# Kernel optimization log

Hardware: AMD Instinct MI355X
Metric: run time of the kernel (lower is better)

## Reference

```python
import jax, jax.numpy as jnp
import numpy as np
from math import erf, pi, sqrt, exp

D = 2048
TARGET_BITS = 2.5
N_HIGH = 1024  # round(D * frac)
N_LOW = D - N_HIGH
HIGH_MSE_BITS = 2  # ceil(2.5) - 1
LOW_MSE_BITS = 1   # floor(2.5) - 1


def _phi(x):
    return np.exp(-0.5 * x * x) / np.sqrt(2.0 * np.pi)


def _Phi(x):
    return 0.5 * (1.0 + np.vectorize(erf)(x / np.sqrt(2.0)))


def lloyd_max_centroids(bits: int) -> np.ndarray:
    """Lloyd-Max optimal scalar quantizer centroids for N(0,1), 2**bits levels."""
    L = 2 ** bits
    c = np.linspace(-2.0, 2.0, L)
    for _ in range(200):
        b = 0.5 * (c[:-1] + c[1:])                      # decision boundaries
        edges = np.concatenate([[-1e9], b, [1e9]])
        lo, hi = edges[:-1], edges[1:]
        mass = _Phi(hi) - _Phi(lo)
        c = (_phi(lo) - _phi(hi)) / np.maximum(mass, 1e-12)  # conditional mean
    return c.astype(np.float32)


def generate_rotation_matrix(d: int, seed: int) -> np.ndarray:
    rng = np.random.default_rng(seed)
    A = rng.standard_normal((d, d)).astype(np.float64)
    Q, R = np.linalg.qr(A)
    Q = Q * np.sign(np.diag(R))[None, :]
    return Q.astype(np.float32)


def setup_inputs() -> dict:
    key = jax.random.key(0)
    kq, kk = jax.random.split(key)
    queries = jax.random.normal(kq, (1024, D), dtype=jnp.float32)
    keys = jax.random.normal(kk, (4096, D), dtype=jnp.float32)
    Pi = jnp.asarray(generate_rotation_matrix(D, seed=42 + 2000))
    high_centroids = jnp.asarray(lloyd_max_centroids(HIGH_MSE_BITS))  # (4,)
    low_centroids = jnp.asarray(lloyd_max_centroids(LOW_MSE_BITS))    # (2,)
    rng = np.random.default_rng(42)
    S_high = jnp.asarray(rng.standard_normal((N_HIGH, N_HIGH)).astype(np.float32))
    rng2 = np.random.default_rng(42 + 1000)
    S_low = jnp.asarray(rng2.standard_normal((N_LOW, N_LOW)).astype(np.float32))
    return {"queries": queries, "keys": keys, "Pi": Pi,
            "high_centroids": high_centroids, "low_centroids": low_centroids,
            "S_high": S_high, "S_low": S_low}


def _quantize_group(y, centroids, S):
    # nearest-centroid scalar quantization per channel
    idx = jnp.argmin(jnp.abs(y[..., None] - centroids), axis=-1)  # (bk, n_ch)
    y_mse = centroids[idx]
    residual = y - y_mse
    residual_norm = jnp.linalg.norm(residual, axis=-1)            # (bk,)
    signs = jnp.sign(residual @ S.T)                              # (bk, m)
    return y_mse, signs, residual_norm


def _ip_group(q_ch, y_mse, signs, residual_norm, S):
    m = S.shape[0]
    term1 = q_ch @ y_mse.T                                        # (bq, bk)
    # QJL estimator: <q, r> ~ sqrt(pi/2)/m * ||r|| * <S q, sign(S r)>
    term2 = (jnp.sqrt(jnp.float32(pi / 2)) / m) * ((q_ch @ S.T) @ signs.T) * residual_norm[None, :]
    return term1 + term2


def reference(queries, keys, Pi, high_centroids, low_centroids, S_high, S_low):
    # ---- quantize keys ----
    vec_norm = jnp.linalg.norm(keys, axis=-1)                     # (bk,)
    k_n = keys / (vec_norm[:, None] + 1e-8)
    y = k_n @ Pi.T
    yh, yl = y[:, :N_HIGH], y[:, N_HIGH:]
    kmse_h, sg_h, rn_h = _quantize_group(yh, high_centroids, S_high)
    kmse_l, sg_l, rn_l = _quantize_group(yl, low_centroids, S_low)
    # ---- inner product estimate ----
    q_rot = queries @ Pi.T
    qh, ql = q_rot[:, :N_HIGH], q_rot[:, N_HIGH:]
    ip = _ip_group(qh, kmse_h, sg_h, rn_h, S_high) + _ip_group(ql, kmse_l, sg_l, rn_l, S_low)
    return ip * vec_norm[None, :]                                 # (bq, bk)
```

## Files before the change

### kernel.cpp

```cpp
#include <hip/hip_runtime.h>
#include <math.h>

#ifndef M_PI
#define M_PI 3.14159265358979323846
#endif

typedef __attribute__((ext_vector_type(8))) __bf16 bf16x8;
typedef __attribute__((ext_vector_type(4))) float f32x4;
typedef __attribute__((ext_vector_type(8))) unsigned short ushort8;
typedef __attribute__((ext_vector_type(4))) unsigned short ushort4v;

__device__ __forceinline__ unsigned short f2bf(float x) {
    unsigned int u = __float_as_uint(x);
    unsigned int r = (u + 0x7FFFu + ((u >> 16) & 1u)) >> 16;
    return (unsigned short)r;
}

__global__ __launch_bounds__(256)
void norm_np_k(const float* __restrict__ keys,
               float* __restrict__ den,
               float* __restrict__ vnorm)
{
#pragma clang fp contract(off)
    const int tid = threadIdx.x;
    const int row_l = tid >> 4;
    const int blk = tid & 15;
    const int row = blockIdx.x * 16 + row_l;
    const float* a = keys + (size_t)row * 2048 + blk * 128;

    float r0 = a[0]*a[0], r1 = a[1]*a[1], r2 = a[2]*a[2], r3 = a[3]*a[3];
    float r4 = a[4]*a[4], r5 = a[5]*a[5], r6 = a[6]*a[6], r7 = a[7]*a[7];
    for (int i = 8; i < 128; i += 8) {
        r0 += a[i+0]*a[i+0]; r1 += a[i+1]*a[i+1];
        r2 += a[i+2]*a[i+2]; r3 += a[i+3]*a[i+3];
        r4 += a[i+4]*a[i+4]; r5 += a[i+5]*a[i+5];
        r6 += a[i+6]*a[i+6]; r7 += a[i+7]*a[i+7];
    }
    float bsum = ((r0 + r1) + (r2 + r3)) + ((r4 + r5) + (r6 + r7));

    __shared__ float bs[16][16];
    bs[row_l][blk] = bsum;
    __syncthreads();
    if (blk == 0) {
        const float* b = bs[row_l];
        float q0 = ((b[0] + b[1]) + (b[2] + b[3])) + ((b[4] + b[5]) + (b[6] + b[7]));
        float q1 = ((b[8] + b[9]) + (b[10] + b[11])) + ((b[12] + b[13]) + (b[14] + b[15]));
        float s = q0 + q1;
        float n = (float)sqrt((double)s);
        den[row] = n + 1e-8f;
        vnorm[row] = n;
    }
}

__global__ __launch_bounds__(256)
void kn_k(const float* __restrict__ keys,
          const float* __restrict__ den,
          float* __restrict__ kn)
{
#pragma clang fp contract(off)
    const int idx = (blockIdx.x * 256 + threadIdx.x) * 8;
    const int row = idx >> 11;
    const float d = den[row];
    float4 v0 = *(const float4*)(keys + idx);
    float4 v1 = *(const float4*)(keys + idx + 4);
    v0.x /= d; v0.y /= d; v0.z /= d; v0.w /= d;
    v1.x /= d; v1.y /= d; v1.z /= d; v1.w /= d;
    *(float4*)(kn + idx) = v0;
    *(float4*)(kn + idx + 4) = v1;
}

__global__ __launch_bounds__(256)
void f2bf_k(const float* __restrict__ in, unsigned short* __restrict__ out)
{
    const int i = (blockIdx.x * 256 + threadIdx.x) * 8;
    float4 v0 = *(const float4*)(in + i);
    float4 v1 = *(const float4*)(in + i + 4);
    ushort8 o;
    o[0] = f2bf(v0.x); o[1] = f2bf(v0.y); o[2] = f2bf(v0.z); o[3] = f2bf(v0.w);
    o[4] = f2bf(v1.x); o[5] = f2bf(v1.y); o[6] = f2bf(v1.z); o[7] = f2bf(v1.w);
    *(ushort8*)(out + i) = o;
}

template <int EPI>
__global__ __launch_bounds__(256)
void gemm_dec_k(const float* __restrict__ A, int lda, int a_zoff,
                const float* __restrict__ B0, const float* __restrict__ B1,
                int ldb,
                float* __restrict__ Cf, unsigned short* __restrict__ Cb,
                int c_zoff, int ldc, int K,
                const float* __restrict__ rv0, const float* __restrict__ rv1)
{
#pragma clang fp contract(off)
    __shared__ float As[16][132];
    __shared__ float Bs[16][132];

    const int z = blockIdx.z;
    const float* Ap = A + (size_t)z * a_zoff;
    const float* Bp = z ? B1 : B0;
    const float* rvp = z ? rv1 : rv0;
    unsigned short* Cbp = (EPI == 1) ? (Cb + (size_t)z * c_zoff) : nullptr;

    const int tid = threadIdx.x;
    const int tr4 = (tid >> 4) * 4;
    const int tc4 = (tid & 15) * 4;
    const int row0 = blockIdx.y * 128;
    const int col0 = blockIdx.x * 128;
    const int sr = tid >> 1;
    const int sk = (tid & 1) * 8;

    const float* ga = Ap + (size_t)(row0 + sr) * lda + sk;
    const float* gb = Bp + (size_t)(col0 + sr) * ldb + sk;

    float acc[2][2][4][4] = {};
    float sa[8], sb[8];

#define LOADSTAGE(off) do { \
    *(float4*)(sa)     = *(const float4*)(ga + (off)); \
    *(float4*)(sa + 4) = *(const float4*)(ga + (off) + 4); \
    *(float4*)(sb)     = *(const float4*)(gb + (off)); \
    *(float4*)(sb + 4) = *(const float4*)(gb + (off) + 4); \
} while (0)

#define RDFRAG(fa, fb, kk) do { \
    *(float4*)(fa)     = *(const float4*)&As[kk][tr4]; \
    *(float4*)(fa + 4) = *(const float4*)&As[kk][tr4 + 64]; \
    *(float4*)(fb)     = *(const float4*)&Bs[kk][tc4]; \
    *(float4*)(fb + 4) = *(const float4*)&Bs[kk][tc4 + 64]; \
} while (0)

#define FMAS(fa, fb) do { \
    _Pragma("unroll") \
    for (int mb = 0; mb < 2; ++mb) \
        _Pragma("unroll") \
        for (int i = 0; i < 4; ++i) \
            _Pragma("unroll") \
            for (int nb = 0; nb < 2; ++nb) \
                _Pragma("unroll") \
                for (int j = 0; j < 4; ++j) \
                    acc[mb][nb][i][j] = fmaf((fa)[mb*4+i], (fb)[nb*4+j], acc[mb][nb][i][j]); \
} while (0)

    LOADSTAGE(0);

    for (int k0 = 0; k0 < K; k0 += 16) {
        __syncthreads();
        #pragma unroll
        for (int u = 0; u < 8; ++u) {
            As[sk + u][sr] = sa[u];
            Bs[sk + u][sr] = sb[u];
        }
        __syncthreads();
        if (k0 + 16 < K) LOADSTAGE(k0 + 16);

        float fa0[8], fb0[8], fa1[8], fb1[8];
        RDFRAG(fa0, fb0, 0);
        #pragma unroll
        for (int kk = 0; kk < 16; kk += 2) {
            RDFRAG(fa1, fb1, kk + 1);
            FMAS(fa0, fb0);
            if (kk + 2 < 16) RDFRAG(fa0, fb0, kk + 2);
            FMAS(fa1, fb1);
        }
    }

    #pragma unroll
    for (int mb = 0; mb < 2; ++mb) {
        #pragma unroll
        for (int i = 0; i < 4; ++i) {
            const int r = row0 + mb * 64 + tr4 + i;
            if (EPI == 0) {
                #pragma unroll
                for (int nb = 0; nb < 2; ++nb)
                    *(float4*)&Cf[(size_t)r * ldc + col0 + nb * 64 + tc4] =
                        *(const float4*)&acc[mb][nb][i][0];
            } else {
                const float s = rvp[r];
                #pragma unroll
                for (int nb = 0; nb < 2; ++nb) {
                    ushort4v o;
                    #pragma unroll
                    for (int j = 0; j < 4; ++j) {
                        const float t = acc[mb][nb][i][j];
                        o[j] = f2bf((t > 0.0f) ? s : ((t < 0.0f) ? -s : 0.0f));
                    }
                    *(ushort4v*)&Cbp[(size_t)r * ldc + col0 + nb * 64 + tc4] = o;
                }
            }
        }
    }
#undef LOADSTAGE
#undef RDFRAG
#undef FMAS
}

__global__ __launch_bounds__(256)
void quant_k(float* __restrict__ Y,
             unsigned short* __restrict__ Bmse,
             const float* __restrict__ ch,
             const float* __restrict__ cl,
             float* __restrict__ sc_h,
             float* __restrict__ sc_l,
             double coefd)
{
#pragma clang fp contract(off)
    const int row = blockIdx.x;
    const int tid = threadIdx.x;
    const int c0 = tid * 8;
    const float h0 = ch[0], h1 = ch[1], h2 = ch[2], h3 = ch[3];
    const float l0 = cl[0], l1 = cl[1];

    float y[8], res[8];
    ushort8 cb;
    *(float4*)(y)     = *(const float4*)(Y + (size_t)row * 2048 + c0);
    *(float4*)(y + 4) = *(const float4*)(Y + (size_t)row * 2048 + c0 + 4);

    const bool high = (tid < 128);
    float ss = 0.0f;
    #pragma unroll
    for (int j = 0; j < 8; ++j) {
        const float v = y[j];
        float cbest;
        if (high) {
            cbest = h0;
            float bd = fabsf(v - h0), dd;
            dd = fabsf(v - h1); if (dd < bd) { bd = dd; cbest = h1; }
            dd = fabsf(v - h2); if (dd < bd) { bd = dd; cbest = h2; }
            dd = fabsf(v - h3); if (dd < bd) { bd = dd; cbest = h3; }
        } else {
            cbest = (fabsf(v - l1) < fabsf(v - l0)) ? l1 : l0;
        }
        res[j] = v - cbest;
        cb[j] = f2bf(cbest);
        ss += res[j] * res[j];
    }
    *(float4*)(Y + (size_t)row * 2048 + c0)     = *(float4*)(res);
    *(float4*)(Y + (size_t)row * 2048 + c0 + 4) = *(float4*)(res + 4);
    *(ushort8*)(Bmse + (size_t)row * 4096 + c0) = cb;

    __shared__ float sm[256];
    sm[tid] = ss;
    __syncthreads();
    for (int o = 64; o > 0; o >>= 1) {
        if ((tid & 127) < o) sm[tid] += sm[tid + o];
        __syncthreads();
    }
    if (tid == 0)   sc_h[row] = (float)(coefd * sqrt((double)sm[0]));
    if (tid == 128) sc_l[row] = (float)(coefd * sqrt((double)sm[128]));
}

template <int EPI>
__global__ __launch_bounds__(256)
void gemm_mfma_k(const unsigned short* __restrict__ A, int lda, int a_zoff,
                 const unsigned short* __restrict__ B0,
                 const unsigned short* __restrict__ B1, int ldb,
                 float* __restrict__ Cf, unsigned short* __restrict__ Cb,
                 int c_zoff, int ldc, int K,
                 const float* __restrict__ colscale)
{
    __shared__ unsigned short As[128][40];
    __shared__ unsigned short Bs[128][40];

    const int z = blockIdx.z;
    const unsigned short* Ap = A + (size_t)z * a_zoff;
    const unsigned short* Bp = z ? B1 : B0;
    unsigned short* Cbp = (EPI == 2) ? (Cb + (size_t)z * c_zoff) : nullptr;

    const int tid = threadIdx.x;
    const int lane = tid & 63;
    const int wid = tid >> 6;
    const int wm = wid >> 1;
    const int wn = wid & 1;
    const int row0 = blockIdx.y * 128;
    const int col0 = blockIdx.x * 128;
    const int sr = tid >> 1;
    const int sk = (tid & 1) * 16;
    const int frow = lane & 15;
    const int fk = (lane >> 4) * 8;

    const unsigned short* ga = Ap + (size_t)(row0 + sr) * lda + sk;
    const unsigned short* gb = Bp + (size_t)(col0 + sr) * ldb + sk;

    f32x4 acc[4][4] = {};

    for (int k0 = 0; k0 < K; k0 += 32) {
        ushort8 a0 = *(const ushort8*)(ga + k0);
        ushort8 a1 = *(const ushort8*)(ga + k0 + 8);
        ushort8 b0 = *(const ushort8*)(gb + k0);
        ushort8 b1 = *(const ushort8*)(gb + k0 + 8);
        __syncthreads();
        *(ushort8*)&As[sr][sk]     = a0;
        *(ushort8*)&As[sr][sk + 8] = a1;
        *(ushort8*)&Bs[sr][sk]     = b0;
        *(ushort8*)&Bs[sr][sk + 8] = b1;
        __syncthreads();

        bf16x8 af[4], bfr[4];
        #pragma unroll
        for (int mi = 0; mi < 4; ++mi)
            af[mi] = *(const bf16x8*)&As[wm * 64 + mi * 16 + frow][fk];
        #pragma unroll
        for (int ni = 0; ni < 4; ++ni)
            bfr[ni] = *(const bf16x8*)&Bs[wn * 64 + ni * 16 + frow][fk];
        #pragma unroll
        for (int mi = 0; mi < 4; ++mi)
            #pragma unroll
            for (int ni = 0; ni < 4; ++ni)
                acc[mi][ni] = __builtin_amdgcn_mfma_f32_16x16x32_bf16(
                    af[mi], bfr[ni], acc[mi][ni], 0, 0, 0);
    }

    const int drow = (lane >> 4) * 4;
    const int dcol = lane & 15;
    #pragma unroll
    for (int mi = 0; mi < 4; ++mi) {
        #pragma unroll
        for (int ni = 0; ni < 4; ++ni) {
            const int c = col0 + wn * 64 + ni * 16 + dcol;
            const float cs = (EPI == 1) ? colscale[c] : 0.0f;
            #pragma unroll
            for (int rg = 0; rg < 4; ++rg) {
                const int r = row0 + wm * 64 + mi * 16 + drow + rg;
                const float v = acc[mi][ni][rg];
                if (EPI == 1) Cf[(size_t)r * ldc + c] = v * cs;
                else          Cbp[(size_t)r * ldc + c] = f2bf(v);
            }
        }
    }
}

extern "C" void kernel_launch(void* const* d_in, const int* in_sizes, int n_in,
                              void* d_out, int out_size, void* d_ws, size_t ws_size,
                              hipStream_t stream)
{
    const float* queries = (const float*)d_in[0];
    const float* keys    = (const float*)d_in[1];
    const float* Pi      = (const float*)d_in[2];
    const float* ch      = (const float*)d_in[3];
    const float* cl      = (const float*)d_in[4];
    const float* S_high  = (const float*)d_in[5];
    const float* S_low   = (const float*)d_in[6];
    float* out = (float*)d_out;

    char* ws = (char*)d_ws;
    float*          kn    = (float*)(ws);
    float*          Y     = (float*)(ws + ((size_t)32 << 20));
    unsigned short* Bbig  = (unsigned short*)(ws + ((size_t)64 << 20));
    unsigned short* Abig  = (unsigned short*)(ws + ((size_t)96 << 20));
    unsigned short* Qb    = (unsigned short*)(ws + ((size_t)104 << 20));
    unsigned short* Pib   = (unsigned short*)(ws + ((size_t)108 << 20));
    unsigned short* Sbh   = (unsigned short*)(ws + ((size_t)116 << 20));
    unsigned short* Sbl   = (unsigned short*)(ws + ((size_t)118 << 20));
    float*          den   = (float*)(ws + ((size_t)120 << 20));
    float*          vnorm = (float*)(ws + ((size_t)120 << 20) + 16384);
    float*          sc_h  = (float*)(ws + ((size_t)120 << 20) + 32768);
    float*          sc_l  = (float*)(ws + ((size_t)120 << 20) + 49152);

    const double coefd = sqrt(M_PI / 2.0) / 1024.0;

    norm_np_k<<<256, 256, 0, stream>>>(keys, den, vnorm);

    kn_k<<<4096, 256, 0, stream>>>(keys, den, kn);

    f2bf_k<<<1024, 256, 0, stream>>>(queries, Qb);
    f2bf_k<<<2048, 256, 0, stream>>>(Pi, Pib);
    f2bf_k<<<512, 256, 0, stream>>>(S_high, Sbh);
    f2bf_k<<<512, 256, 0, stream>>>(S_low, Sbl);

    gemm_dec_k<0><<<dim3(16, 32, 1), 256, 0, stream>>>(
        kn, 2048, 0, Pi, Pi, 2048, Y, nullptr, 0, 2048, 2048, nullptr, nullptr);

    quant_k<<<4096, 256, 0, stream>>>(Y, Bbig, ch, cl, sc_h, sc_l, coefd);

    gemm_dec_k<1><<<dim3(8, 32, 2), 256, 0, stream>>>(
        Y, 2048, 1024, S_high, S_low, 1024,
        nullptr, Bbig + 2048, 1024, 4096, 1024, sc_h, sc_l);

    gemm_mfma_k<2><<<dim3(16, 8, 1), 256, 0, stream>>>(
        Qb, 2048, 0, Pib, Pib, 2048, nullptr, Abig, 0, 4096, 2048, nullptr);
    gemm_mfma_k<2><<<dim3(8, 8, 2), 256, 0, stream>>>(
        Abig, 4096, 1024, Sbh, Sbl, 1024, nullptr, Abig + 2048, 1024, 4096, 1024, nullptr);

    gemm_mfma_k<1><<<dim3(32, 8, 1), 256, 0, stream>>>(
        Abig, 4096, 0, Bbig, Bbig, 4096, out, nullptr, 0, 4096, 4096, vnorm);
}
```

Before: 829.2 us.

## Double-buffer LDS tiles and use packed FP32 FMA in the fp32 GEMM

The fp32 SIMT GEMM now keeps two LDS buffers, so the next K-slice is written to the alternate buffer after compute and only one barrier is needed per iteration instead of two. The inner product loop is rewritten with inline v_pk_fma_f32 asm, where each instruction updates two accumulators, which roughly halves the FMA instruction count. The risks are doubled LDS use, which may lower occupancy, and inline asm that can block compiler scheduling. Rounding stays the same because each result is still a single fused multiply-add.

```diff
diff --git a/kernel.cpp b/kernel.cpp
--- a/kernel.cpp
+++ b/kernel.cpp
@@ -7,6 +7,7 @@
 
 typedef __attribute__((ext_vector_type(8))) __bf16 bf16x8;
 typedef __attribute__((ext_vector_type(4))) float f32x4;
+typedef __attribute__((ext_vector_type(2))) float f32x2;
 typedef __attribute__((ext_vector_type(8))) unsigned short ushort8;
 typedef __attribute__((ext_vector_type(4))) unsigned short ushort4v;
 
@@ -15,6 +16,13 @@
     unsigned int r = (u + 0x7FFFu + ((u >> 16) & 1u)) >> 16;
     return (unsigned short)r;
 }
+
+#define PKFMA_L(d, a, b) \
+    asm("v_pk_fma_f32 %0, %1, %2, %0 op_sel:[0,0,0] op_sel_hi:[0,1,1]" \
+        : "+v"(d) : "v"(a), "v"(b))
+#define PKFMA_H(d, a, b) \
+    asm("v_pk_fma_f32 %0, %1, %2, %0 op_sel:[1,0,0] op_sel_hi:[1,1,1]" \
+        : "+v"(d) : "v"(a), "v"(b))
 
 __global__ __launch_bounds__(256)
 void norm_np_k(const float* __restrict__ keys,
@@ -91,8 +99,8 @@
                 const float* __restrict__ rv0, const float* __restrict__ rv1)
 {
 #pragma clang fp contract(off)
-    __shared__ float As[16][132];
-    __shared__ float Bs[16][132];
+    __shared__ float As[2][16][132];
+    __shared__ float Bs[2][16][132];
 
     const int z = blockIdx.z;
     const float* Ap = A + (size_t)z * a_zoff;
@@ -111,7 +119,7 @@
     const float* ga = Ap + (size_t)(row0 + sr) * lda + sk;
     const float* gb = Bp + (size_t)(col0 + sr) * ldb + sk;
 
-    float acc[2][2][4][4] = {};
+    f32x2 acc[8][4] = {};
     float sa[8], sb[8];
 
 #define LOADSTAGE(off) do { \
@@ -121,74 +129,86 @@
     *(float4*)(sb + 4) = *(const float4*)(gb + (off) + 4); \
 } while (0)
 
-#define RDFRAG(fa, fb, kk) do { \
-    *(float4*)(fa)     = *(const float4*)&As[kk][tr4]; \
-    *(float4*)(fa + 4) = *(const float4*)&As[kk][tr4 + 64]; \
-    *(float4*)(fb)     = *(const float4*)&Bs[kk][tc4]; \
-    *(float4*)(fb + 4) = *(const float4*)&Bs[kk][tc4 + 64]; \
+#define STORESTAGE(buf) do { \
+    _Pragma("unroll") \
+    for (int u = 0; u < 8; ++u) { \
+        As[buf][sk + u][sr] = sa[u]; \
+        Bs[buf][sk + u][sr] = sb[u]; \
+    } \
+} while (0)
+
+#define RDFRAG(fa, fb, kk, buf) do { \
+    float4 va0 = *(const float4*)&As[buf][kk][tr4]; \
+    float4 va1 = *(const float4*)&As[buf][kk][tr4 + 64]; \
+    float4 vb0 = *(const float4*)&Bs[buf][kk][tc4]; \
+    float4 vb1 = *(const float4*)&Bs[buf][kk][tc4 + 64]; \
+    (fa)[0] = (f32x2){va0.x, va0.y}; (fa)[1] = (f32x2){va0.z, va0.w}; \
+    (fa)[2] = (f32x2){va1.x, va1.y}; (fa)[3] = (f32x2){va1.z, va1.w}; \
+    (fb)[0] = (f32x2){vb0.x, vb0.y}; (fb)[1] = (f32x2){vb0.z, vb0.w}; \
+    (fb)[2] = (f32x2){vb1.x, vb1.y}; (fb)[3] = (f32x2){vb1.z, vb1.w}; \
 } while (0)
 
 #define FMAS(fa, fb) do { \
     _Pragma("unroll") \
-    for (int mb = 0; mb < 2; ++mb) \
+    for (int p = 0; p < 4; ++p) { \
         _Pragma("unroll") \
-        for (int i = 0; i < 4; ++i) \
-            _Pragma("unroll") \
-            for (int nb = 0; nb < 2; ++nb) \
-                _Pragma("unroll") \
-                for (int j = 0; j < 4; ++j) \
-                    acc[mb][nb][i][j] = fmaf((fa)[mb*4+i], (fb)[nb*4+j], acc[mb][nb][i][j]); \
+        for (int q = 0; q < 4; ++q) { \
+            PKFMA_L(acc[2*p][q],   (fa)[p], (fb)[q]); \
+            PKFMA_H(acc[2*p+1][q], (fa)[p], (fb)[q]); \
+        } \
+    } \
 } while (0)
 
     LOADSTAGE(0);
+    STORESTAGE(0);
+    __syncthreads();
+    int cur = 0;
 
     for (int k0 = 0; k0 < K; k0 += 16) {
-        __syncthreads();
-        #pragma unroll
-        for (int u = 0; u < 8; ++u) {
-            As[sk + u][sr] = sa[u];
-            Bs[sk + u][sr] = sb[u];
-        }
-        __syncthreads();
-        if (k0 + 16 < K) LOADSTAGE(k0 + 16);
-
-        float fa0[8], fb0[8], fa1[8], fb1[8];
-        RDFRAG(fa0, fb0, 0);
+        const bool more = (k0 + 16 < K);
+        if (more) LOADSTAGE(k0 + 16);
+
+        f32x2 fa0[4], fb0[4], fa1[4], fb1[4];
+        RDFRAG(fa0, fb0, 0, cur);
         #pragma unroll
         for (int kk = 0; kk < 16; kk += 2) {
-            RDFRAG(fa1, fb1, kk + 1);
+            RDFRAG(fa1, fb1, kk + 1, cur);
             FMAS(fa0, fb0);
-            if (kk + 2 < 16) RDFRAG(fa0, fb0, kk + 2);
+            if (kk + 2 < 16) RDFRAG(fa0, fb0, kk + 2, cur);
             FMAS(fa1, fb1);
         }
+
+        if (more) STORESTAGE(cur ^ 1);
+        __syncthreads();
+        cur ^= 1;
     }
 
     #pragma unroll
-    for (int mb = 0; mb < 2; ++mb) {
-        #pragma unroll
-        for (int i = 0; i < 4; ++i) {
-            const int r = row0 + mb * 64 + tr4 + i;
-            if (EPI == 0) {
-                #pragma unroll
-                for (int nb = 0; nb < 2; ++nb)
-                    *(float4*)&Cf[(size_t)r * ldc + col0 + nb * 64 + tc4] =
-                        *(const float4*)&acc[mb][nb][i][0];
-            } else {
-                const float s = rvp[r];
-                #pragma unroll
-                for (int nb = 0; nb < 2; ++nb) {
-                    ushort4v o;
-                    #pragma unroll
-                    for (int j = 0; j < 4; ++j) {
-                        const float t = acc[mb][nb][i][j];
-                        o[j] = f2bf((t > 0.0f) ? s : ((t < 0.0f) ? -s : 0.0f));
-                    }
-                    *(ushort4v*)&Cbp[(size_t)r * ldc + col0 + nb * 64 + tc4] = o;
-                }
+    for (int ai = 0; ai < 8; ++ai) {
+        const int r = row0 + ((ai < 4) ? (tr4 + ai) : (64 + tr4 + ai - 4));
+        if (EPI == 0) {
+            float4 lo4 = {acc[ai][0].x, acc[ai][0].y, acc[ai][1].x, acc[ai][1].y};
+            float4 hi4 = {acc[ai][2].x, acc[ai][2].y, acc[ai][3].x, acc[ai][3].y};
+            *(float4*)&Cf[(size_t)r * ldc + col0 + tc4]      = lo4;
+            *(float4*)&Cf[(size_t)r * ldc + col0 + 64 + tc4] = hi4;
+        } else {
+            const float s = rvp[r];
+            float v[8] = {acc[ai][0].x, acc[ai][0].y, acc[ai][1].x, acc[ai][1].y,
+                          acc[ai][2].x, acc[ai][2].y, acc[ai][3].x, acc[ai][3].y};
+            ushort4v o0, o1;
+            #pragma unroll
+            for (int j = 0; j < 4; ++j) {
+                const float t0 = v[j];
+                o0[j] = f2bf((t0 > 0.0f) ? s : ((t0 < 0.0f) ? -s : 0.0f));
+                const float t1 = v[4 + j];
+                o1[j] = f2bf((t1 > 0.0f) ? s : ((t1 < 0.0f) ? -s : 0.0f));
             }
+            *(ushort4v*)&Cbp[(size_t)r * ldc + col0 + tc4]      = o0;
+            *(ushort4v*)&Cbp[(size_t)r * ldc + col0 + 64 + tc4] = o1;
         }
     }
 #undef LOADSTAGE
+#undef STORESTAGE
 #undef RDFRAG
 #undef FMAS
 }
```

Result: faster. 800.4 us (-3.5%).

## Rewrite fp32 decode GEMM with packed FMA, register-direct A loads, double-buffered B

Applied to the files above, without the earlier changes.

Restructures the fp32 GEMM used for rotation and sign projection. A fragments now load straight from global memory into registers with a software double buffer, and only B is staged through LDS. That LDS tile is double-buffered with a 32-wide K step, so there is one barrier per step instead of two. The inner product uses inline v_pk_fma_f32 on float pairs to halve FMA instruction count, and launch bounds request 2 waves per SIMD. The cost is higher register pressure and uncoalesced per-row A loads, and the inline asm bypasses the fp contract(off) intent, though FMA semantics are unchanged.

```diff
diff --git a/kernel.cpp b/kernel.cpp
--- a/kernel.cpp
+++ b/kernel.cpp
@@ -7,6 +7,7 @@
 
 typedef __attribute__((ext_vector_type(8))) __bf16 bf16x8;
 typedef __attribute__((ext_vector_type(4))) float f32x4;
+typedef __attribute__((ext_vector_type(2))) float f32x2;
 typedef __attribute__((ext_vector_type(8))) unsigned short ushort8;
 typedef __attribute__((ext_vector_type(4))) unsigned short ushort4v;
 
@@ -15,6 +16,13 @@
     unsigned int r = (u + 0x7FFFu + ((u >> 16) & 1u)) >> 16;
     return (unsigned short)r;
 }
+
+#define PKFMA_L(d, a, b) \
+    asm("v_pk_fma_f32 %0, %1, %2, %0 op_sel:[0,0,0] op_sel_hi:[0,1,1]" \
+        : "+v"(d) : "v"(a), "v"(b))
+#define PKFMA_H(d, a, b) \
+    asm("v_pk_fma_f32 %0, %1, %2, %0 op_sel:[1,0,0] op_sel_hi:[1,1,1]" \
+        : "+v"(d) : "v"(a), "v"(b))
 
 __global__ __launch_bounds__(256)
 void norm_np_k(const float* __restrict__ keys,
@@ -82,7 +90,7 @@
 }
 
 template <int EPI>
-__global__ __launch_bounds__(256)
+__global__ __launch_bounds__(256, 2)
 void gemm_dec_k(const float* __restrict__ A, int lda, int a_zoff,
                 const float* __restrict__ B0, const float* __restrict__ B1,
                 int ldb,
@@ -91,8 +99,7 @@
                 const float* __restrict__ rv0, const float* __restrict__ rv1)
 {
 #pragma clang fp contract(off)
-    __shared__ float As[16][132];
-    __shared__ float Bs[16][132];
+    __shared__ float Bs[2][32][132];
 
     const int z = blockIdx.z;
     const float* Ap = A + (size_t)z * a_zoff;
@@ -105,92 +112,109 @@
     const int tc4 = (tid & 15) * 4;
     const int row0 = blockIdx.y * 128;
     const int col0 = blockIdx.x * 128;
-    const int sr = tid >> 1;
-    const int sk = (tid & 1) * 8;
-
-    const float* ga = Ap + (size_t)(row0 + sr) * lda + sk;
-    const float* gb = Bp + (size_t)(col0 + sr) * ldb + sk;
-
-    float acc[2][2][4][4] = {};
-    float sa[8], sb[8];
-
-#define LOADSTAGE(off) do { \
-    *(float4*)(sa)     = *(const float4*)(ga + (off)); \
-    *(float4*)(sa + 4) = *(const float4*)(ga + (off) + 4); \
-    *(float4*)(sb)     = *(const float4*)(gb + (off)); \
-    *(float4*)(sb + 4) = *(const float4*)(gb + (off) + 4); \
+    const int sc  = tid >> 1;
+    const int skb = (tid & 1) * 16;
+
+    const float* gb = Bp + (size_t)(col0 + sc) * ldb + skb;
+
+    const float* garow[8];
+    #pragma unroll
+    for (int i = 0; i < 4; ++i) {
+        garow[i]     = Ap + (size_t)(row0 + tr4 + i) * lda;
+        garow[4 + i] = Ap + (size_t)(row0 + 64 + tr4 + i) * lda;
+    }
+
+    f32x2 acc[8][4] = {};
+    f32x2 agA[16], agB[16];
+    float sb[16];
+
+#define ALOAD(dst, koff) do { \
+    _Pragma("unroll") \
+    for (int r = 0; r < 8; ++r) \
+        *(float4*)&dst[2 * r] = *(const float4*)(garow[r] + (koff)); \
 } while (0)
 
-#define RDFRAG(fa, fb, kk) do { \
-    *(float4*)(fa)     = *(const float4*)&As[kk][tr4]; \
-    *(float4*)(fa + 4) = *(const float4*)&As[kk][tr4 + 64]; \
-    *(float4*)(fb)     = *(const float4*)&Bs[kk][tc4]; \
-    *(float4*)(fb + 4) = *(const float4*)&Bs[kk][tc4 + 64]; \
+#define BLOADG(koff) do { \
+    *(float4*)(sb)      = *(const float4*)(gb + (koff)); \
+    *(float4*)(sb + 4)  = *(const float4*)(gb + (koff) + 4); \
+    *(float4*)(sb + 8)  = *(const float4*)(gb + (koff) + 8); \
+    *(float4*)(sb + 12) = *(const float4*)(gb + (koff) + 12); \
 } while (0)
 
-#define FMAS(fa, fb) do { \
+#define BSTORE(buf) do { \
     _Pragma("unroll") \
-    for (int mb = 0; mb < 2; ++mb) \
-        _Pragma("unroll") \
-        for (int i = 0; i < 4; ++i) \
-            _Pragma("unroll") \
-            for (int nb = 0; nb < 2; ++nb) \
-                _Pragma("unroll") \
-                for (int j = 0; j < 4; ++j) \
-                    acc[mb][nb][i][j] = fmaf((fa)[mb*4+i], (fb)[nb*4+j], acc[mb][nb][i][j]); \
+    for (int u = 0; u < 16; ++u) Bs[buf][skb + u][sc] = sb[u]; \
 } while (0)
 
-    LOADSTAGE(0);
-
-    for (int k0 = 0; k0 < K; k0 += 16) {
-        __syncthreads();
+    BLOADG(0);
+    BSTORE(0);
+    ALOAD(agA, 0);
+    __syncthreads();
+    int cur = 0;
+
+    for (int k0 = 0; k0 < K; k0 += 32) {
+        const bool moreP = (k0 + 32 < K);
+        if (moreP) BLOADG(k0 + 32);
+
         #pragma unroll
-        for (int u = 0; u < 8; ++u) {
-            As[sk + u][sr] = sa[u];
-            Bs[sk + u][sr] = sb[u];
-        }
-        __syncthreads();
-        if (k0 + 16 < K) LOADSTAGE(k0 + 16);
-
-        float fa0[8], fb0[8], fa1[8], fb1[8];
-        RDFRAG(fa0, fb0, 0);
-        #pragma unroll
-        for (int kk = 0; kk < 16; kk += 2) {
-            RDFRAG(fa1, fb1, kk + 1);
-            FMAS(fa0, fb0);
-            if (kk + 2 < 16) RDFRAG(fa0, fb0, kk + 2);
-            FMAS(fa1, fb1);
-        }
-    }
-
-    #pragma unroll
-    for (int mb = 0; mb < 2; ++mb) {
-        #pragma unroll
-        for (int i = 0; i < 4; ++i) {
-            const int r = row0 + mb * 64 + tr4 + i;
-            if (EPI == 0) {
+        for (int g = 0; g < 8; ++g) {
+            const int nko = k0 + (g + 1) * 4;
+            if ((g & 1) == 0) { if (nko < K) ALOAD(agB, nko); }
+            else              { if (nko < K) ALOAD(agA, nko); }
+            const f32x2* acur = (g & 1) ? agB : agA;
+
+            #pragma unroll
+            for (int j = 0; j < 4; ++j) {
+                const int kk = g * 4 + j;
+                float4 vb0 = *(const float4*)&Bs[cur][kk][tc4];
+                float4 vb1 = *(const float4*)&Bs[cur][kk][tc4 + 64];
+                f32x2 fb[4];
+                fb[0] = (f32x2){vb0.x, vb0.y}; fb[1] = (f32x2){vb0.z, vb0.w};
+                fb[2] = (f32x2){vb1.x, vb1.y}; fb[3] = (f32x2){vb1.z, vb1.w};
                 #pragma unroll
-                for (int nb = 0; nb < 2; ++nb)
-                    *(float4*)&Cf[(size_t)r * ldc + col0 + nb * 64 + tc4] =
-                        *(const float4*)&acc[mb][nb][i][0];
-            } else {
-                const float s = rvp[r];
-                #pragma unroll
-                for (int nb = 0; nb < 2; ++nb) {
-                    ushort4v o;
+                for (int r = 0; r < 8; ++r) {
+                    const f32x2 ap = acur[2 * r + (j >> 1)];
                     #pragma unroll
-                    for (int j = 0; j < 4; ++j) {
-                        const float t = acc[mb][nb][i][j];
-                        o[j] = f2bf((t > 0.0f) ? s : ((t < 0.0f) ? -s : 0.0f));
+                    for (int q = 0; q < 4; ++q) {
+                        if (j & 1) { PKFMA_H(acc[r][q], ap, fb[q]); }
+                        else       { PKFMA_L(acc[r][q], ap, fb[q]); }
                     }
-                    *(ushort4v*)&Cbp[(size_t)r * ldc + col0 + nb * 64 + tc4] = o;
                 }
             }
         }
-    }
-#undef LOADSTAGE
-#undef RDFRAG
-#undef FMAS
+
+        if (moreP) BSTORE(cur ^ 1);
+        __syncthreads();
+        cur ^= 1;
+    }
+
+    #pragma unroll
+    for (int r = 0; r < 8; ++r) {
+        const int row = row0 + ((r < 4) ? (tr4 + r) : (64 + tr4 + r - 4));
+        if (EPI == 0) {
+            float4 lo4 = {acc[r][0].x, acc[r][0].y, acc[r][1].x, acc[r][1].y};
+            float4 hi4 = {acc[r][2].x, acc[r][2].y, acc[r][3].x, acc[r][3].y};
+            *(float4*)&Cf[(size_t)row * ldc + col0 + tc4]      = lo4;
+            *(float4*)&Cf[(size_t)row * ldc + col0 + 64 + tc4] = hi4;
+        } else {
+            const float s = rvp[row];
+            float v[8] = {acc[r][0].x, acc[r][0].y, acc[r][1].x, acc[r][1].y,
+                          acc[r][2].x, acc[r][2].y, acc[r][3].x, acc[r][3].y};
+            ushort4v o0, o1;
+            #pragma unroll
+            for (int j = 0; j < 4; ++j) {
+                const float t0 = v[j];
+                o0[j] = f2bf((t0 > 0.0f) ? s : ((t0 < 0.0f) ? -s : 0.0f));
+                const float t1 = v[4 + j];
+                o1[j] = f2bf((t1 > 0.0f) ? s : ((t1 < 0.0f) ? -s : 0.0f));
+            }
+            *(ushort4v*)&Cbp[(size_t)row * ldc + col0 + tc4]      = o0;
+            *(ushort4v*)&Cbp[(size_t)row * ldc + col0 + 64 + tc4] = o1;
+        }
+    }
+#undef ALOAD
+#undef BLOADG
+#undef BSTORE
 }
 
 __global__ __launch_bounds__(256)
```

After: 864.2 us. +4.2%, slower.
